# Kernel optimization log

Measured on AMD Instinct MI355X. Metric: run time of the kernel, lower is better.

Reference implementation:

```python
import jax, jax.numpy as jnp
import numpy as np

S, B, D, H = 2048, 2, 1024, 16
DK = D // H
SCALE = 1.0 / np.sqrt(DK)


def setup_inputs() -> dict:
    key = jax.random.key(0)
    ks = jax.random.split(key, 8)
    return {
        "query": jax.random.normal(ks[0], (S, B, D), dtype=jnp.float32),
        "key": jax.random.normal(ks[1], (S, B, D), dtype=jnp.float32),
        "value": jax.random.normal(ks[2], (S, B, D), dtype=jnp.float32),
        "mask": jax.random.randint(ks[3], (B, S, S), 0, 2, dtype=jnp.int32),
        "in_proj_weight": jax.random.normal(ks[4], (3 * D, D), dtype=jnp.float32) * 0.02,
        "in_proj_bias": jax.random.normal(ks[5], (3 * D,), dtype=jnp.float32) * 0.02,
        "out_proj_weight": jax.random.normal(ks[6], (D, D), dtype=jnp.float32) * 0.02,
        "out_proj_bias": jax.random.normal(ks[7], (D,), dtype=jnp.float32) * 0.02,
    }


def reference(query, key, value, mask, in_proj_weight, in_proj_bias,
              out_proj_weight, out_proj_bias):
    seq_len, batch, d_model = query.shape
    # split fused in-projection: order is query, key, value
    Wq, Wk, Wv = in_proj_weight[:D], in_proj_weight[D:2 * D], in_proj_weight[2 * D:]
    bq, bk, bv = in_proj_bias[:D], in_proj_bias[D:2 * D], in_proj_bias[2 * D:]
    # PrepareForMultiHeadAttention: x @ W^T + b, then split heads -> [s, b, h, d_k]
    q = (query @ Wq.T + bq).reshape(seq_len, batch, H, DK)
    k = (key @ Wk.T + bk).reshape(key.shape[0], batch, H, DK)
    v = (value @ Wv.T + bv).reshape(value.shape[0], batch, H, DK)
    # scores [i, j, b, h] in float32, scaled
    scores = jnp.einsum('ibhd,jbhd->ijbh', q, k).astype(jnp.float32) * SCALE
    # mask: [b, q, k] -> permute(1,2,0) -> [q, k, b] -> unsqueeze(-1)
    m = jnp.transpose(mask, (1, 2, 0))[..., None]
    scores = jnp.where(m == 1, jnp.float32(-1e9), scores)
    # softmax over key axis (dim=1)
    attn = jax.nn.softmax(scores, axis=1)
    # dropout p=0.0 -> identity
    x = jnp.einsum('ijbh,jbhd->ibhd', attn, v).reshape(seq_len, batch, -1)
    return x @ out_proj_weight.T + out_proj_bias
```

## Files before the change

### kernel.cpp

```cpp
#include <hip/hip_runtime.h>
#include <hip/hip_bf16.h>

typedef unsigned short u16;
typedef unsigned int   u32;
typedef unsigned long long u64;
typedef __bf16 bf16x8 __attribute__((ext_vector_type(8)));
typedef float  f32x4  __attribute__((ext_vector_type(4)));

#define S_LEN  2048
#define BATCH  2
#define DMODEL 1024
#define NHEADS 16
#define DKH    64
#define MWORDS (S_LEN/64)
#define SCALE_LOG2E 0.18033688011112042f

__device__ __forceinline__ u16 f2bf(float f){
  u32 x = __builtin_bit_cast(u32, f);
  x += 0x7fffu + ((x >> 16) & 1u);
  return (u16)(x >> 16);
}
__device__ __forceinline__ bf16x8 ld8(const u16* p){ return *(const bf16x8*)p; }

__device__ __forceinline__ u32 pk_bf16(float a, float b){
  u32 d;
  asm("v_cvt_pk_bf16_f32 %0, %1, %2" : "=v"(d) : "v"(a), "v"(b));
  return d;
}

__device__ __forceinline__ u32 bitmask32(u32 v, int i){
#if __has_builtin(__builtin_amdgcn_sbfe)
  return (u32)__builtin_amdgcn_sbfe((int)v, (u32)i, 1u);
#else
  return 0u - ((v >> i) & 1u);
#endif
}

__device__ __forceinline__ void gload16(const u16* g, u16* l){
  __builtin_amdgcn_global_load_lds(
      (const __attribute__((address_space(1))) u32*)(u64)g,
      (__attribute__((address_space(3))) u32*)(u64)l,
      16, 0, 0);
}

__global__ __launch_bounds__(256) void cvt_kernel(
    const float* __restrict__ a0, const float* __restrict__ a1, const float* __restrict__ a2,
    const float* __restrict__ wi, const float* __restrict__ wo, const int* __restrict__ msk,
    u16* __restrict__ d0, u16* __restrict__ d1, u16* __restrict__ d2,
    u16* __restrict__ dwi, u16* __restrict__ dwo, u64* __restrict__ mbits)
{
  int tid = blockIdx.x*256 + threadIdx.x;
  int stride = gridDim.x*256;
  const int NX = S_LEN*BATCH*DMODEL/4;
  for (int i = tid; i < NX; i += stride){
    f32x4 x0 = ((const f32x4*)a0)[i];
    f32x4 x1 = ((const f32x4*)a1)[i];
    f32x4 x2 = ((const f32x4*)a2)[i];
    ((ushort4*)d0)[i] = make_ushort4(f2bf(x0[0]), f2bf(x0[1]), f2bf(x0[2]), f2bf(x0[3]));
    ((ushort4*)d1)[i] = make_ushort4(f2bf(x1[0]), f2bf(x1[1]), f2bf(x1[2]), f2bf(x1[3]));
    ((ushort4*)d2)[i] = make_ushort4(f2bf(x2[0]), f2bf(x2[1]), f2bf(x2[2]), f2bf(x2[3]));
  }
  const int NWI = 3*DMODEL*DMODEL/4;
  for (int i = tid; i < NWI; i += stride){
    f32x4 x = ((const f32x4*)wi)[i];
    ((ushort4*)dwi)[i] = make_ushort4(f2bf(x[0]), f2bf(x[1]), f2bf(x[2]), f2bf(x[3]));
  }
  const int NWO = DMODEL*DMODEL/4;
  for (int i = tid; i < NWO; i += stride){
    f32x4 x = ((const f32x4*)wo)[i];
    ((ushort4*)dwo)[i] = make_ushort4(f2bf(x[0]), f2bf(x[1]), f2bf(x[2]), f2bf(x[3]));
  }
  int gw   = tid >> 6;
  int lane = threadIdx.x & 63;
  int nwaves = stride >> 6;
  const int NW = BATCH*S_LEN*MWORDS;
  for (int w4 = gw*4; w4 < NW; w4 += nwaves*4){
    int v0 = msk[(size_t)(w4+0)*64 + lane];
    int v1 = msk[(size_t)(w4+1)*64 + lane];
    int v2 = msk[(size_t)(w4+2)*64 + lane];
    int v3 = msk[(size_t)(w4+3)*64 + lane];
    u64 b0 = __ballot(v0 == 0);
    u64 b1 = __ballot(v1 == 0);
    u64 b2 = __ballot(v2 == 0);
    u64 b3 = __ballot(v3 == 0);
    if (lane == 0){
      mbits[w4+0] = b0; mbits[w4+1] = b1;
      mbits[w4+2] = b2; mbits[w4+3] = b3;
    }
  }
}

__device__ __forceinline__ void gemm128_loop(
    const u16* __restrict__ A, const u16* __restrict__ W,
    u16* abuf, u16* bbuf, int tid, f32x4 acc[4][4])
{
  int lane = tid & 63, quad = lane >> 4, r = lane & 15;
  int wv = tid >> 6, wm = (wv & 1)*64, wn = (wv >> 1)*64;
  int c0 = tid, c1 = tid + 256;
  int r0 = c0 >> 2, g0 = ((c0 & 3) ^ (r0 & 3))*8;
  int r1 = c1 >> 2, g1 = ((c1 & 3) ^ (r1 & 3))*8;
  const u16* ga0 = A + (size_t)r0*DMODEL + g0;
  const u16* ga1 = A + (size_t)r1*DMODEL + g1;
  const u16* gb0 = W + (size_t)r0*DMODEL + g0;
  const u16* gb1 = W + (size_t)r1*DMODEL + g1;
  int sw = (quad ^ (r & 3))*8;

  auto stage = [&](int bu, int k0){
    u16* ab = abuf + bu*(128*32);
    u16* bb = bbuf + bu*(128*32);
    gload16(ga0 + k0, ab + c0*8);
    gload16(ga1 + k0, ab + c1*8);
    gload16(gb0 + k0, bb + c0*8);
    gload16(gb1 + k0, bb + c1*8);
  };
  auto step = [&](int bu){
    const u16* ab = abuf + bu*(128*32);
    const u16* bb = bbuf + bu*(128*32);
    bf16x8 af[4], bfr[4];
    #pragma unroll
    for (int i = 0; i < 4; ++i) af[i]  = ld8(&ab[(wm + i*16 + r)*32 + sw]);
    #pragma unroll
    for (int i = 0; i < 4; ++i) bfr[i] = ld8(&bb[(wn + i*16 + r)*32 + sw]);
    #pragma unroll
    for (int mi = 0; mi < 4; ++mi)
      #pragma unroll
      for (int ni = 0; ni < 4; ++ni)
        acc[mi][ni] = __builtin_amdgcn_mfma_f32_16x16x32_bf16(af[mi], bfr[ni], acc[mi][ni], 0,0,0);
  };

  stage(0, 0);
  __syncthreads();
  for (int k0 = 0; k0 < DMODEL; k0 += 64){
    stage(1, k0 + 32);
    step(0);
    __syncthreads();
    if (k0 + 64 < DMODEL) stage(0, k0 + 64);
    step(1);
    __syncthreads();
  }
}

__global__ __launch_bounds__(256) void qkv_proj_kernel(
    const u16* __restrict__ xq, const u16* __restrict__ xk, const u16* __restrict__ xv,
    const u16* __restrict__ w, const float* __restrict__ bias,
    u16* __restrict__ q_ws, u16* __restrict__ k_ws, u16* __restrict__ vt_ws)
{
  __shared__ __align__(16) u16 abuf[2*128*32];
  __shared__ __align__(16) u16 bbuf[2*128*32];
  int tid = threadIdx.x;
  int lane = tid & 63, quad = lane >> 4, r = lane & 15;
  int wv = tid >> 6, wm = (wv & 1)*64, wn = (wv >> 1)*64;
  int m0 = blockIdx.x*128, n0 = blockIdx.y*128;
  int t = n0 >> 10;
  const u16* X = (t == 0) ? xq : (t == 1) ? xk : xv;

  f32x4 acc[4][4] = {};
  gemm128_loop(X + (size_t)m0*DMODEL, w + (size_t)n0*DMODEL, abuf, bbuf, tid, acc);

  int mbase = m0 + wm, nbase = n0 + wn;
  #pragma unroll
  for (int ni = 0; ni < 4; ++ni){
    int n  = nbase + ni*16 + r;
    float bv = bias[n];
    int nn = n & (DMODEL-1);
    int h = nn >> 6, dk = nn & 63;
    #pragma unroll
    for (int mi = 0; mi < 4; ++mi){
      #pragma unroll
      for (int reg = 0; reg < 4; ++reg){
        int m = mbase + mi*16 + quad*4 + reg;
        int s = m >> 1, b = m & 1;
        u16 hv = f2bf(acc[mi][ni][reg] + bv);
        size_t bh = (size_t)(b*NHEADS + h);
        if (t == 0)      q_ws [(bh*S_LEN + s)*DKH + dk] = hv;
        else if (t == 1) k_ws [(bh*S_LEN + s)*DKH + dk] = hv;
        else             vt_ws[(bh*DKH + dk)*S_LEN + s] = hv;
      }
    }
  }
}

__global__ __launch_bounds__(512) void attn_kernel(
    const u16* __restrict__ q_ws, const u16* __restrict__ k_ws, const u16* __restrict__ vt_ws,
    const u64* __restrict__ mbits, u16* __restrict__ x_ws)
{
  __shared__ __align__(16) u16 kbuf[2][64*64];
  __shared__ __align__(16) u16 vbuf[2][64*64];
  __shared__ __align__(16) u16 pbuf[8][16*64];
  int tid  = threadIdx.x;
  int wv   = tid >> 6;
  int lane = tid & 63;
  int quad = lane >> 4, r = lane & 15;

  int lin  = blockIdx.y * 16 + blockIdx.x;
  int xcd  = lin & 7, slot = lin >> 3;
  int bh   = (xcd << 2) | (slot >> 4);
  int xt   = slot & 15;
  int b  = bh >> 4, h = bh & 15;
  int i0 = (xt*8 + wv) * 16;

  const u16* Q  = q_ws  + (size_t)bh*S_LEN*DKH;
  const u16* K  = k_ws  + (size_t)bh*S_LEN*DKH;
  const u16* Vt = vt_ws + (size_t)bh*DKH*S_LEN;
  const u64* MB = mbits + ((size_t)b*S_LEN + (i0 + r))*MWORDS;

  int sr  = tid >> 3;
  int sc8 = (tid & 7) * 8;
  int ssw = ((tid & 7) ^ (sr & 7)) * 8;
  const u16* Kp = K  + (size_t)sr*DKH   + sc8;
  const u16* Vp = Vt + (size_t)sr*S_LEN + sc8;

  const u16* qrow = Q + (size_t)(i0 + r)*DKH + quad*8;
  bf16x8 qf0 = ld8(qrow), qf1 = ld8(qrow + 32);

  int m7   = r & 7;
  int ksw0 = (quad ^ m7) * 8;
  int ksw1 = ksw0 ^ 32;
  int pw0  = ((quad >> 1) ^ m7) * 8 + (quad & 1)*4;

  float l_part = 0.f;
  f32x4 o[4] = {};
  f32x4 z = {0.f, 0.f, 0.f, 0.f};
  u16* pl = pbuf[wv];

  bf16x8 ka_, va_, kb_, vb_;
  auto loadset = [&](bf16x8& kv, bf16x8& vv, int j0){
    kv = ld8(Kp + (size_t)j0*DKH);
    vv = ld8(Vp + j0);
  };
  auto storeset = [&](int bu, bf16x8 kv, bf16x8 vv){
    *(bf16x8*)&kbuf[bu][sr*64 + ssw] = kv;
    *(bf16x8*)&vbuf[bu][sr*64 + ssw] = vv;
  };
  auto compute = [&](int bu, u64 mb){
    const u16* kb = kbuf[bu];
    const u16* vb = vbuf[bu];
    float p[16];
    #pragma unroll
    for (int c = 0; c < 4; ++c){
      int rowb = (16*c + r)*64;
      bf16x8 ka = ld8(&kb[rowb + ksw0]);
      bf16x8 k8 = ld8(&kb[rowb + ksw1]);
      __builtin_amdgcn_s_setprio(1);
      f32x4 s = __builtin_amdgcn_mfma_f32_16x16x32_bf16(ka, qf0, z, 0,0,0);
      s       = __builtin_amdgcn_mfma_f32_16x16x32_bf16(k8, qf1, s, 0,0,0);
      __builtin_amdgcn_s_setprio(0);
      u32 mc = (u32)(mb >> (16*c + 4*quad));
      #pragma unroll
      for (int i = 0; i < 4; ++i){
        float ev = __builtin_amdgcn_exp2f(s[i]*SCALE_LOG2E);
        p[c*4+i] = __builtin_bit_cast(float,
                     __builtin_bit_cast(u32, ev) & bitmask32(mc, i));
        l_part += p[c*4+i];
      }
    }
    #pragma unroll
    for (int c = 0; c < 4; ++c){
      u32 k0 = pk_bf16(p[c*4+0], p[c*4+1]);
      u32 k1 = pk_bf16(p[c*4+2], p[c*4+3]);
      *(uint2*)&pl[r*64 + ((pw0 & ~7) ^ (2*c*8)) + (pw0 & 7)] = make_uint2(k0, k1);
    }
    asm volatile("s_waitcnt lgkmcnt(0)" ::: "memory");
    bf16x8 pf0 = ld8(&pl[r*64 + ksw0]);
    bf16x8 pf1 = ld8(&pl[r*64 + ksw1]);
    __builtin_amdgcn_s_setprio(1);
    #pragma unroll
    for (int tt = 0; tt < 4; ++tt){
      int rowb = (tt*16 + r)*64;
      bf16x8 va = ld8(&vb[rowb + ksw0]);
      bf16x8 v8 = ld8(&vb[rowb + ksw1]);
      o[tt] = __builtin_amdgcn_mfma_f32_16x16x32_bf16(pf0, va, o[tt], 0,0,0);
      o[tt] = __builtin_amdgcn_mfma_f32_16x16x32_bf16(pf1, v8, o[tt], 0,0,0);
    }
    __builtin_amdgcn_s_setprio(0);
  };

  loadset(ka_, va_, 0);
  storeset(0, ka_, va_);
  loadset(kb_, vb_, 64);
  __syncthreads();

  for (int j0 = 0; j0 < S_LEN; j0 += 128){
    storeset(1, kb_, vb_);
    if (j0 + 128 < S_LEN) loadset(ka_, va_, j0 + 128);
    compute(0, MB[j0 >> 6]);
    __syncthreads();
    if (j0 + 128 < S_LEN) storeset(0, ka_, va_);
    if (j0 + 192 < S_LEN) loadset(kb_, vb_, j0 + 192);
    compute(1, MB[(j0 >> 6) + 1]);
    __syncthreads();
  }

  l_part += __shfl_xor(l_part, 16, 64);
  l_part += __shfl_xor(l_part, 32, 64);
  float l0 = 1.f/__shfl(l_part, quad*4+0, 64);
  float l1 = 1.f/__shfl(l_part, quad*4+1, 64);
  float l2 = 1.f/__shfl(l_part, quad*4+2, 64);
  float l3 = 1.f/__shfl(l_part, quad*4+3, 64);
  #pragma unroll
  for (int tt = 0; tt < 4; ++tt){
    int col = h*DKH + tt*16 + r;
    x_ws[((size_t)(i0 + quad*4 + 0)*BATCH + b)*DMODEL + col] = f2bf(o[tt][0]*l0);
    x_ws[((size_t)(i0 + quad*4 + 1)*BATCH + b)*DMODEL + col] = f2bf(o[tt][1]*l1);
    x_ws[((size_t)(i0 + quad*4 + 2)*BATCH + b)*DMODEL + col] = f2bf(o[tt][2]*l2);
    x_ws[((size_t)(i0 + quad*4 + 3)*BATCH + b)*DMODEL + col] = f2bf(o[tt][3]*l3);
  }
}

__global__ __launch_bounds__(256) void out_proj_kernel(
    const u16* __restrict__ x, const u16* __restrict__ w, const float* __restrict__ bias,
    float* __restrict__ out)
{
  __shared__ __align__(16) u16 abuf[2*128*32];
  __shared__ __align__(16) u16 bbuf[2*128*32];
  int tid = threadIdx.x;
  int lane = tid & 63, quad = lane >> 4, r = lane & 15;
  int wv = tid >> 6, wm = (wv & 1)*64, wn = (wv >> 1)*64;
  int m0 = blockIdx.x*128, n0 = blockIdx.y*128;

  f32x4 acc[4][4] = {};
  gemm128_loop(x + (size_t)m0*DMODEL, w + (size_t)n0*DMODEL, abuf, bbuf, tid, acc);

  int mbase = m0 + wm, nbase = n0 + wn;
  #pragma unroll
  for (int ni = 0; ni < 4; ++ni){
    int n = nbase + ni*16 + r;
    float bv = bias[n];
    #pragma unroll
    for (int mi = 0; mi < 4; ++mi){
      #pragma unroll
      for (int reg = 0; reg < 4; ++reg){
        int m = mbase + mi*16 + quad*4 + reg;
        out[(size_t)m*DMODEL + n] = acc[mi][ni][reg] + bv;
      }
    }
  }
}

extern "C" void kernel_launch(void* const* d_in, const int* in_sizes, int n_in,
                              void* d_out, int out_size, void* d_ws, size_t ws_size,
                              hipStream_t stream) {
  (void)in_sizes; (void)n_in; (void)out_size; (void)ws_size;
  const float* query = (const float*)d_in[0];
  const float* key   = (const float*)d_in[1];
  const float* value = (const float*)d_in[2];
  const int*   mask  = (const int*)d_in[3];
  const float* w_in  = (const float*)d_in[4];
  const float* b_in  = (const float*)d_in[5];
  const float* w_out = (const float*)d_in[6];
  const float* b_out = (const float*)d_in[7];
  float* out = (float*)d_out;

  const size_t TSZ = (size_t)BATCH*NHEADS*S_LEN*DKH;
  const size_t XSZ = (size_t)S_LEN*BATCH*DMODEL;
  u16* q_ws  = (u16*)d_ws;
  u16* k_ws  = q_ws  + TSZ;
  u16* vt_ws = k_ws  + TSZ;
  u16* x_ws  = vt_ws + TSZ;
  u16* xq_bf = x_ws  + XSZ;
  u16* xk_bf = xq_bf + XSZ;
  u16* xv_bf = xk_bf + XSZ;
  u16* wi_bf = xv_bf + XSZ;
  u16* wo_bf = wi_bf + (size_t)3*DMODEL*DMODEL;
  u64* mb_ws = (u64*)(wo_bf + (size_t)DMODEL*DMODEL);

  cvt_kernel<<<1024, 256, 0, stream>>>(query, key, value, w_in, w_out, mask,
                                       xq_bf, xk_bf, xv_bf, wi_bf, wo_bf, mb_ws);
  qkv_proj_kernel<<<dim3(32, 24), 256, 0, stream>>>(xq_bf, xk_bf, xv_bf, wi_bf, b_in,
                                                    q_ws, k_ws, vt_ws);
  attn_kernel<<<dim3(16, 32), 512, 0, stream>>>(q_ws, k_ws, vt_ws, mb_ws, x_ws);
  out_proj_kernel<<<dim3(32, 8), 256, 0, stream>>>(x_ws, wo_bf, b_out, out);
}
```

Before: 257.0 us.

## Split attention key range across two wave groups per block and merge partials

The attention block grows to 1024 threads, and two groups of 8 waves each process half of the key sequence for the same query rows. Each group streams K/V in 32-key tiles through its own double-buffered shared memory region, then the second group writes its partial outputs and row sums to shared memory for the first group to merge and normalize. This raises the number of waves per block to hide latency on the serial key loop. In exchange it adds a shared-memory reduction, smaller MFMA tiles per barrier, and more block-wide synchronization, and register pressure grows under the 1024-thread launch bound.

```diff
diff --git a/kernel.cpp b/kernel.cpp
--- a/kernel.cpp
+++ b/kernel.cpp
@@ -180,17 +180,18 @@
   }
 }
 
-__global__ __launch_bounds__(512) void attn_kernel(
+__global__ __launch_bounds__(1024, 8) void attn_kernel(
     const u16* __restrict__ q_ws, const u16* __restrict__ k_ws, const u16* __restrict__ vt_ws,
     const u64* __restrict__ mbits, u16* __restrict__ x_ws)
 {
-  __shared__ __align__(16) u16 kbuf[2][64*64];
-  __shared__ __align__(16) u16 vbuf[2][64*64];
-  __shared__ __align__(16) u16 pbuf[8][16*64];
+  __shared__ __align__(16) u16 smem[3*8192];
   int tid  = threadIdx.x;
-  int wv   = tid >> 6;
+  int wv16 = tid >> 6;
+  int z    = wv16 >> 3;
+  int wv   = wv16 & 7;
   int lane = tid & 63;
   int quad = lane >> 4, r = lane & 15;
+  int kz   = z << 10;
 
   int lin  = blockIdx.y * 16 + blockIdx.x;
   int xcd  = lin & 7, slot = lin >> 3;
@@ -204,48 +205,53 @@
   const u16* Vt = vt_ws + (size_t)bh*DKH*S_LEN;
   const u64* MB = mbits + ((size_t)b*S_LEN + (i0 + r))*MWORDS;
 
-  int sr  = tid >> 3;
-  int sc8 = (tid & 7) * 8;
-  int ssw = ((tid & 7) ^ (sr & 7)) * 8;
-  const u16* Kp = K  + (size_t)sr*DKH   + sc8;
-  const u16* Vp = Vt + (size_t)sr*S_LEN + sc8;
+  int lt   = tid & 511;
+  bool isK = lt < 256;
+  int krow = lt >> 3,  kch = lt & 7;
+  int vl   = lt & 255;
+  int vrow = vl >> 3 ? vl >> 2 : vl >> 2;
+  vrow = vl >> 2;  int vch = vl & 3;
+  const u16* gK = K  + (size_t)krow*DKH   + kch*8;
+  const u16* gV = Vt + (size_t)vrow*S_LEN + vch*8;
+  u16* kbz = smem          + (z*2)*2048;
+  u16* vbz = smem + 8192   + (z*2)*2048;
+  u16* ldst0 = isK ? (kbz + krow*64 + ((kch ^ (krow & 7))*8))
+                   : (vbz + vrow*32 + ((vch ^ (vrow & 3))*8));
+  u16* ldst1 = ldst0 + 2048;
 
   const u16* qrow = Q + (size_t)(i0 + r)*DKH + quad*8;
   bf16x8 qf0 = ld8(qrow), qf1 = ld8(qrow + 32);
 
-  int m7   = r & 7;
+  int m7   = r & 7, m3 = r & 3;
   int ksw0 = (quad ^ m7) * 8;
   int ksw1 = ksw0 ^ 32;
-  int pw0  = ((quad >> 1) ^ m7) * 8 + (quad & 1)*4;
+  int psw  = (quad ^ m3) * 8;
+  int pwh  = (quad & 1) * 4;
+  int pwq  = quad >> 1;
 
   float l_part = 0.f;
   f32x4 o[4] = {};
-  f32x4 z = {0.f, 0.f, 0.f, 0.f};
-  u16* pl = pbuf[wv];
-
-  bf16x8 ka_, va_, kb_, vb_;
-  auto loadset = [&](bf16x8& kv, bf16x8& vv, int j0){
-    kv = ld8(Kp + (size_t)j0*DKH);
-    vv = ld8(Vp + j0);
+  f32x4 z4 = {0.f, 0.f, 0.f, 0.f};
+  u16* pl = smem + 16384 + wv16*512;
+
+  bf16x8 sa, sb;
+  auto gload = [&](int kbase)->bf16x8 {
+    return isK ? ld8(gK + (size_t)kbase*DKH) : ld8(gV + kbase);
   };
-  auto storeset = [&](int bu, bf16x8 kv, bf16x8 vv){
-    *(bf16x8*)&kbuf[bu][sr*64 + ssw] = kv;
-    *(bf16x8*)&vbuf[bu][sr*64 + ssw] = vv;
-  };
-  auto compute = [&](int bu, u64 mb){
-    const u16* kb = kbuf[bu];
-    const u16* vb = vbuf[bu];
-    float p[16];
-    #pragma unroll
-    for (int c = 0; c < 4; ++c){
+  auto compute = [&](int bu, u64 mb, int sh){
+    const u16* kb = kbz + bu*2048;
+    const u16* vb = vbz + bu*2048;
+    float p[8];
+    #pragma unroll
+    for (int c = 0; c < 2; ++c){
       int rowb = (16*c + r)*64;
       bf16x8 ka = ld8(&kb[rowb + ksw0]);
       bf16x8 k8 = ld8(&kb[rowb + ksw1]);
       __builtin_amdgcn_s_setprio(1);
-      f32x4 s = __builtin_amdgcn_mfma_f32_16x16x32_bf16(ka, qf0, z, 0,0,0);
+      f32x4 s = __builtin_amdgcn_mfma_f32_16x16x32_bf16(ka, qf0, z4, 0,0,0);
       s       = __builtin_amdgcn_mfma_f32_16x16x32_bf16(k8, qf1, s, 0,0,0);
       __builtin_amdgcn_s_setprio(0);
-      u32 mc = (u32)(mb >> (16*c + 4*quad));
+      u32 mc = (u32)(mb >> (sh + 16*c + 4*quad));
       #pragma unroll
       for (int i = 0; i < 4; ++i){
         float ev = __builtin_amdgcn_exp2f(s[i]*SCALE_LOG2E);
@@ -255,55 +261,75 @@
       }
     }
     #pragma unroll
-    for (int c = 0; c < 4; ++c){
+    for (int c = 0; c < 2; ++c){
       u32 k0 = pk_bf16(p[c*4+0], p[c*4+1]);
       u32 k1 = pk_bf16(p[c*4+2], p[c*4+3]);
-      *(uint2*)&pl[r*64 + ((pw0 & ~7) ^ (2*c*8)) + (pw0 & 7)] = make_uint2(k0, k1);
+      int pwc = (2*c + pwq) ^ m3;
+      *(uint2*)&pl[r*32 + pwc*8 + pwh] = make_uint2(k0, k1);
     }
     asm volatile("s_waitcnt lgkmcnt(0)" ::: "memory");
-    bf16x8 pf0 = ld8(&pl[r*64 + ksw0]);
-    bf16x8 pf1 = ld8(&pl[r*64 + ksw1]);
+    bf16x8 pf = ld8(&pl[r*32 + psw]);
     __builtin_amdgcn_s_setprio(1);
     #pragma unroll
     for (int tt = 0; tt < 4; ++tt){
-      int rowb = (tt*16 + r)*64;
-      bf16x8 va = ld8(&vb[rowb + ksw0]);
-      bf16x8 v8 = ld8(&vb[rowb + ksw1]);
-      o[tt] = __builtin_amdgcn_mfma_f32_16x16x32_bf16(pf0, va, o[tt], 0,0,0);
-      o[tt] = __builtin_amdgcn_mfma_f32_16x16x32_bf16(pf1, v8, o[tt], 0,0,0);
+      bf16x8 vf = ld8(&vb[(tt*16 + r)*32 + psw]);
+      o[tt] = __builtin_amdgcn_mfma_f32_16x16x32_bf16(pf, vf, o[tt], 0,0,0);
     }
     __builtin_amdgcn_s_setprio(0);
   };
 
-  loadset(ka_, va_, 0);
-  storeset(0, ka_, va_);
-  loadset(kb_, vb_, 64);
+  sa = gload(kz);
+  *(bf16x8*)ldst0 = sa;
+  sb = gload(kz + 32);
   __syncthreads();
 
-  for (int j0 = 0; j0 < S_LEN; j0 += 128){
-    storeset(1, kb_, vb_);
-    if (j0 + 128 < S_LEN) loadset(ka_, va_, j0 + 128);
-    compute(0, MB[j0 >> 6]);
+  for (int j0 = 0; j0 < 1024; j0 += 64){
+    u64 mb = MB[(kz + j0) >> 6];
+    *(bf16x8*)ldst1 = sb;
+    if (j0 + 64 < 1024) sa = gload(kz + j0 + 64);
+    compute(0, mb, 0);
     __syncthreads();
-    if (j0 + 128 < S_LEN) storeset(0, ka_, va_);
-    if (j0 + 192 < S_LEN) loadset(kb_, vb_, j0 + 192);
-    compute(1, MB[(j0 >> 6) + 1]);
+    if (j0 + 64 < 1024) *(bf16x8*)ldst0 = sa;
+    if (j0 + 96 < 1024) sb = gload(kz + j0 + 96);
+    compute(1, mb, 32);
     __syncthreads();
   }
 
   l_part += __shfl_xor(l_part, 16, 64);
   l_part += __shfl_xor(l_part, 32, 64);
-  float l0 = 1.f/__shfl(l_part, quad*4+0, 64);
-  float l1 = 1.f/__shfl(l_part, quad*4+1, 64);
-  float l2 = 1.f/__shfl(l_part, quad*4+2, 64);
-  float l3 = 1.f/__shfl(l_part, quad*4+3, 64);
-  #pragma unroll
-  for (int tt = 0; tt < 4; ++tt){
-    int col = h*DKH + tt*16 + r;
-    x_ws[((size_t)(i0 + quad*4 + 0)*BATCH + b)*DMODEL + col] = f2bf(o[tt][0]*l0);
-    x_ws[((size_t)(i0 + quad*4 + 1)*BATCH + b)*DMODEL + col] = f2bf(o[tt][1]*l1);
-    x_ws[((size_t)(i0 + quad*4 + 2)*BATCH + b)*DMODEL + col] = f2bf(o[tt][2]*l2);
-    x_ws[((size_t)(i0 + quad*4 + 3)*BATCH + b)*DMODEL + col] = f2bf(o[tt][3]*l3);
+
+  float* osc = (float*)smem;
+  float* lsc = (float*)(smem + 16384);
+  if (z == 1){
+    float* sl = osc + wv*1024;
+    #pragma unroll
+    for (int tt = 0; tt < 4; ++tt)
+      #pragma unroll
+      for (int reg = 0; reg < 4; ++reg)
+        sl[(quad*4 + reg)*64 + tt*16 + r] = o[tt][reg];
+    if (quad == 0) lsc[wv*16 + r] = l_part;
+  }
+  __syncthreads();
+  if (z == 0){
+    float* sl = osc + wv*1024;
+    #pragma unroll
+    for (int tt = 0; tt < 4; ++tt)
+      #pragma unroll
+      for (int reg = 0; reg < 4; ++reg)
+        o[tt][reg] += sl[(quad*4 + reg)*64 + tt*16 + r];
+    float lt_ = l_part + lsc[wv*16 + r];
+    float l0 = 1.f/__shfl(lt_, quad*4+0, 64);
+    float l1 = 1.f/__shfl(lt_, quad*4+1, 64);
+    float l2 = 1.f/__shfl(lt_, quad*4+2, 64);
+    float l3 = 1.f/__shfl(lt_, quad*4+3, 64);
+    #pragma unroll
+    for (int tt = 0; tt < 4; ++tt){
+      int col = h*DKH + tt*16 + r;
+      x_ws[((size_t)(i0 + quad*4 + 0)*BATCH + b)*DMODEL + col] = f2bf(o[tt][0]*l0);
+      x_ws[((size_t)(i0 + quad*4 + 1)*BATCH + b)*DMODEL + col] = f2bf(o[tt][1]*l1);
+      x_ws[((size_t)(i0 + quad*4 + 2)*BATCH + b)*DMODEL + col] = f2bf(o[tt][2]*l2);
+      x_ws[((size_t)(i0 + quad*4 + 3)*BATCH + b)*DMODEL + col] = f2bf(o[tt][3]*l3);
+    }
   }
 }
 
@@ -368,6 +394,6 @@
                                        xq_bf, xk_bf, xv_bf, wi_bf, wo_bf, mb_ws);
   qkv_proj_kernel<<<dim3(32, 24), 256, 0, stream>>>(xq_bf, xk_bf, xv_bf, wi_bf, b_in,
                                                     q_ws, k_ws, vt_ws);
-  attn_kernel<<<dim3(16, 32), 512, 0, stream>>>(q_ws, k_ws, vt_ws, mb_ws, x_ws);
+  attn_kernel<<<dim3(16, 32), 1024, 0, stream>>>(q_ws, k_ws, vt_ws, mb_ws, x_ws);
   out_proj_kernel<<<dim3(32, 8), 256, 0, stream>>>(x_ws, wo_bf, b_out, out);
 }
```

Measured after the change: 300.1 us. 1.17x slower.
